# Performance work log

Measured on AMD Instinct MI355X. Metric: run time of the kernel, lower is better.

Reference implementation:

```python
import jax, jax.numpy as jnp
import numpy as np

B, L, D_MODEL, H = 2, 2048, 1024, 16
HD = D_MODEL // H  # head dim = 64


def setup_inputs() -> dict:
    key = jax.random.key(0)
    ks = jax.random.split(key, 11)
    s = 1.0 / np.sqrt(D_MODEL)
    inp = {
        "Q": jax.random.normal(ks[0], (B, L, D_MODEL), jnp.float32),
        "K": jax.random.normal(ks[1], (B, L, D_MODEL), jnp.float32),
        "V": jax.random.normal(ks[2], (B, L, D_MODEL), jnp.float32),
        "Wq": jax.random.normal(ks[3], (D_MODEL, D_MODEL), jnp.float32) * s,
        "bq": jnp.zeros((D_MODEL,), jnp.float32),
        "Wk": jax.random.normal(ks[4], (D_MODEL, D_MODEL), jnp.float32) * s,
        "bk": jnp.zeros((D_MODEL,), jnp.float32),
        "Wv": jax.random.normal(ks[5], (D_MODEL, D_MODEL), jnp.float32) * s,
        "bv": jnp.zeros((D_MODEL,), jnp.float32),
        "Wo": jax.random.normal(ks[6], (D_MODEL, D_MODEL), jnp.float32) * s,
        "bo": jnp.zeros((D_MODEL,), jnp.float32),
    }
    return inp


def _split_heads(x):
    # [B, L, H*D] -> [B, H, L, D]
    return x.reshape(B, L, H, HD).transpose(0, 2, 1, 3)


def reference(Q, K, V, Wq, bq, Wk, bk, Wv, bv, Wo, bo):
    q = _split_heads(Q @ Wq.T + bq)
    k = _split_heads(K @ Wk.T + bk)
    v = _split_heads(V @ Wv.T + bv)
    scale = 1.0 / jnp.sqrt(jnp.asarray(HD, q.dtype))
    # full [B, H, L, L] score matrix, as in the original bmm->softmax->bmm
    scores = jnp.einsum("bhqd,bhkd->bhqk", q, k) * scale
    attn = jax.nn.softmax(scores, axis=-1)
    o = jnp.einsum("bhqk,bhkd->bhqd", attn, v)
    o = o.transpose(0, 2, 1, 3).reshape(B, L, D_MODEL)  # concat heads
    return o @ Wo.T + bo
```

## Files before the change

### kernel.cpp

```cpp
#include <hip/hip_runtime.h>
#include <math.h>
#include <stdint.h>

typedef __bf16 bf16_t;
typedef __attribute__((ext_vector_type(2))) __bf16 bf16x2;
typedef __attribute__((ext_vector_type(8))) __bf16 bf16x8;
typedef __attribute__((ext_vector_type(4))) float f32x4;
typedef __attribute__((ext_vector_type(16))) float f32x16;
typedef __attribute__((address_space(1))) unsigned int gu32;
typedef __attribute__((address_space(3))) unsigned int lu32;

#define MFMA16(a, b, c) __builtin_amdgcn_mfma_f32_16x16x32_bf16((a), (b), (c), 0, 0, 0)
#define MFMA32(a, b, c) __builtin_amdgcn_mfma_f32_32x32x16_bf16((a), (b), (c), 0, 0, 0)

__device__ __forceinline__ void gll16(const void* g, void* l) {
    __builtin_amdgcn_global_load_lds((const gu32*)(uintptr_t)g,
                                     (lu32*)(uintptr_t)l, 16, 0, 0);
}

__device__ __forceinline__ bf16x8 ld_frag68(const bf16_t* p) {
    union { bf16x8 v; uint2 u[2]; } r;
    r.u[0] = *(const uint2*)p;
    r.u[1] = *(const uint2*)(p + 4);
    return r.v;
}

__global__ __launch_bounds__(256) void convert_all(
    const float* __restrict__ Q, const float* __restrict__ K, const float* __restrict__ V,
    const float* __restrict__ Wq, const float* __restrict__ Wk, const float* __restrict__ Wv,
    const float* __restrict__ Wo, bf16_t* __restrict__ dst) {
    size_t e0 = (size_t)blockIdx.x * 2048;
    const float* src; size_t off;
    if (e0 < 4194304)       { src = Q;  off = e0; }
    else if (e0 < 8388608)  { src = K;  off = e0 - 4194304; }
    else if (e0 < 12582912) { src = V;  off = e0 - 8388608; }
    else if (e0 < 13631488) { src = Wq; off = e0 - 12582912; }
    else if (e0 < 14680064) { src = Wk; off = e0 - 13631488; }
    else if (e0 < 15728640) { src = Wv; off = e0 - 14680064; }
    else                    { src = Wo; off = e0 - 15728640; }
#pragma unroll
    for (int p = 0; p < 2; ++p) {
        int t = p * 1024 + threadIdx.x * 4;
        float4 v = *(const float4*)(src + off + t);
        union { ushort4 u; bf16_t h[4]; } pk;
        pk.h[0] = (bf16_t)v.x; pk.h[1] = (bf16_t)v.y;
        pk.h[2] = (bf16_t)v.z; pk.h[3] = (bf16_t)v.w;
        *(ushort4*)(dst + e0 + t) = pk.u;
    }
}

__global__ __launch_bounds__(256) void qkv_gemm(
    const bf16_t* __restrict__ Qb, const bf16_t* __restrict__ Kb, const bf16_t* __restrict__ Vb,
    const bf16_t* __restrict__ Wqb, const bf16_t* __restrict__ Wkb, const bf16_t* __restrict__ Wvb,
    const float* __restrict__ bq, const float* __restrict__ bk, const float* __restrict__ bv,
    bf16_t* __restrict__ qo, bf16_t* __restrict__ ko, bf16_t* __restrict__ vT) {
    constexpr int Kdim = 1024, N = 1024;
    __shared__ __attribute__((aligned(16))) bf16_t smem[2 * 128 * 64];
    bf16_t* As = smem;
    bf16_t* Bs = smem + 128 * 64;

    const int tid = threadIdx.x, wave = tid >> 6, lane = tid & 63;
    const int z = blockIdx.z;
    const bf16_t* A = (z == 0) ? Qb : (z == 1) ? Kb : Vb;
    const bf16_t* W = (z == 0) ? Wqb : (z == 1) ? Wkb : Wvb;
    const float* bias = (z == 0) ? bq : (z == 1) ? bk : bv;
    const int bm = blockIdx.x * 128, bn = blockIdx.y * 128;
    const int l16 = lane & 15, quad = lane >> 4;
    const int wm = (wave >> 1) * 64, wn = (wave & 1) * 64;
    const int grow = lane >> 3, gcol = (lane & 7) * 8;

    f32x4 acc[4][4] = {};

    for (int k0 = 0; k0 < Kdim; k0 += 64) {
#pragma unroll
        for (int j = 0; j < 4; ++j) {
            int chunk = wave * 4 + j;
            int row = chunk * 8 + grow;
            gll16(A + (size_t)(bm + row) * Kdim + k0 + gcol, As + chunk * 512);
            gll16(W + (size_t)(bn + row) * Kdim + k0 + gcol, Bs + chunk * 512);
        }
        __syncthreads();
#pragma unroll
        for (int ks = 0; ks < 64; ks += 32) {
            bf16x8 af[4], bf[4];
#pragma unroll
            for (int i = 0; i < 4; ++i)
                af[i] = *(const bf16x8*)&As[(wm + i * 16 + l16) * 64 + ks + quad * 8];
#pragma unroll
            for (int i = 0; i < 4; ++i)
                bf[i] = *(const bf16x8*)&Bs[(wn + i * 16 + l16) * 64 + ks + quad * 8];
#pragma unroll
            for (int i = 0; i < 4; ++i)
#pragma unroll
                for (int j = 0; j < 4; ++j)
                    acc[i][j] = MFMA16(af[i], bf[j], acc[i][j]);
        }
        __syncthreads();
    }

    if (z < 2) {
        bf16_t* outp = (z == 0) ? qo : ko;
        const float sc = (z == 0) ? 0.18033688011112042f : 1.0f;
        constexpr int RST = 132;
#pragma unroll
        for (int p = 0; p < 2; ++p) {
            __syncthreads();
            if ((wave >> 1) == p) {
#pragma unroll
                for (int mi = 0; mi < 4; ++mi)
#pragma unroll
                    for (int nj = 0; nj < 4; ++nj) {
                        int col = wn + nj * 16 + l16;
                        float bv_ = bias[bn + col];
#pragma unroll
                        for (int r = 0; r < 4; ++r) {
                            int rp = mi * 16 + quad * 4 + r;
                            smem[rp * RST + col] = (bf16_t)((acc[mi][nj][r] + bv_) * sc);
                        }
                    }
            }
            __syncthreads();
            int rp = tid >> 2;
            int cb = (tid & 3) * 32;
            int row = bm + p * 64 + rp;
            int srow = row;
            if (z == 1) {
                int w = row & 63;
                srow = (row & ~63) | ((w & 1) ? 32 + (w >> 1) : (w >> 1));
            }
#pragma unroll
            for (int j = 0; j < 4; ++j) {
                uint2 lo = *(const uint2*)&smem[rp * RST + cb + j * 8];
                uint2 hi = *(const uint2*)&smem[rp * RST + cb + j * 8 + 4];
                *(uint4*)&outp[(size_t)srow * N + bn + cb + j * 8] =
                    make_uint4(lo.x, lo.y, hi.x, hi.y);
            }
        }
    } else {
#pragma unroll
        for (int mi = 0; mi < 4; ++mi)
#pragma unroll
            for (int nj = 0; nj < 4; ++nj) {
                int col = bn + wn + nj * 16 + l16;
                int h = col >> 6, d = col & 63;
                float bv_ = bias[col];
                int row0 = bm + wm + mi * 16 + quad * 4;
                int bb = row0 >> 11, l = row0 & 2047;
                union { ushort4 u; bf16_t h4[4]; } pk;
#pragma unroll
                for (int r = 0; r < 4; ++r) pk.h4[r] = (bf16_t)(acc[mi][nj][r] + bv_);
                *(ushort4*)&vT[(((size_t)bb * 16 + h) * 64 + d) * 2048 + l] = pk.u;
            }
    }
}

__global__ __launch_bounds__(256) void out_gemm(const bf16_t* __restrict__ A,
                                                const bf16_t* __restrict__ W,
                                                const float* __restrict__ bias,
                                                float* __restrict__ out) {
    constexpr int Kdim = 1024, N = 1024;
    __shared__ __attribute__((aligned(16))) bf16_t As[64 * 64];
    __shared__ __attribute__((aligned(16))) bf16_t Bs[128 * 64];
    const int tid = threadIdx.x, wave = tid >> 6, lane = tid & 63;
    const int bm = blockIdx.x * 64, bn = blockIdx.y * 128;
    const int l16 = lane & 15, quad = lane >> 4;
    const int wm = (wave >> 1) * 32, wn = (wave & 1) * 64;
    const int grow = lane >> 3, gcol = (lane & 7) * 8;
    f32x4 acc[2][4] = {};

    for (int k0 = 0; k0 < Kdim; k0 += 64) {
#pragma unroll
        for (int j = 0; j < 2; ++j) {
            int chunk = wave * 2 + j;
            int row = chunk * 8 + grow;
            gll16(A + (size_t)(bm + row) * Kdim + k0 + gcol, As + chunk * 512);
        }
#pragma unroll
        for (int j = 0; j < 4; ++j) {
            int chunk = wave * 4 + j;
            int row = chunk * 8 + grow;
            gll16(W + (size_t)(bn + row) * Kdim + k0 + gcol, Bs + chunk * 512);
        }
        __syncthreads();
#pragma unroll
        for (int ks = 0; ks < 64; ks += 32) {
            bf16x8 af[2], bf[4];
#pragma unroll
            for (int i = 0; i < 2; ++i)
                af[i] = *(const bf16x8*)&As[(wm + i * 16 + l16) * 64 + ks + quad * 8];
#pragma unroll
            for (int i = 0; i < 4; ++i)
                bf[i] = *(const bf16x8*)&Bs[(wn + i * 16 + l16) * 64 + ks + quad * 8];
#pragma unroll
            for (int i = 0; i < 2; ++i)
#pragma unroll
                for (int j = 0; j < 4; ++j)
                    acc[i][j] = MFMA16(af[i], bf[j], acc[i][j]);
        }
        __syncthreads();
    }
#pragma unroll
    for (int mi = 0; mi < 2; ++mi)
#pragma unroll
        for (int nj = 0; nj < 4; ++nj) {
            int col = bn + wn + nj * 16 + l16;
            float bv_ = bias[col];
#pragma unroll
            for (int r = 0; r < 4; ++r) {
                int row = bm + wm + mi * 16 + quad * 4 + r;
                out[(size_t)row * N + col] = acc[mi][nj][r] + bv_;
            }
        }
}

__global__ __launch_bounds__(256, 4) void attn5(const bf16_t* __restrict__ qo,
                                                const bf16_t* __restrict__ ko,
                                                const bf16_t* __restrict__ vT,
                                                bf16_t* __restrict__ Op,
                                                float* __restrict__ lpp) {
    constexpr int L = 2048, D = 1024, ST = 68;
    __shared__ __attribute__((aligned(16))) bf16_t ksm[64 * ST];
    __shared__ __attribute__((aligned(16))) bf16_t vsm[64 * ST];
    __shared__ __attribute__((aligned(16))) bf16_t psm[4][32 * ST];

    const int tid = threadIdx.x, wave = tid >> 6, lane = tid & 63;
    const int l31 = lane & 31, hi = lane >> 5;
    const int b = blockIdx.x >> 4, h = blockIdx.x & 15;
    const int q0 = blockIdx.y * 128;
    const int split = blockIdx.z;
    bf16_t* pw = psm[wave];
    bf16_t* Opart = Op + (size_t)split * 4194304;
    float* lpart = lpp + split * 65536;

    const int rloc = tid >> 2, cg = tid & 3;
    const bf16_t* kbase = ko + ((size_t)b * L + rloc) * D + h * 64 + cg * 16;
    const bf16_t* vbase = vT + (((size_t)b * 16 + h) * 64 + rloc) * L + cg * 16;

    bf16x8 qf[4];
    {
        const bf16_t* qptr = qo + ((size_t)b * L + q0 + wave * 32 + l31) * D + h * 64 + hi * 8;
#pragma unroll
        for (int ks = 0; ks < 4; ++ks) qf[ks] = *(const bf16x8*)(qptr + ks * 16);
    }

    f32x16 o0{}, o1{};
    float lp[16];
#pragma unroll
    for (int r = 0; r < 16; ++r) lp[r] = 0.f;

    const int kt0 = split * 16, kt1 = kt0 + 16;
    for (int kt = kt0; kt < kt1; ++kt) {
        const size_t koff = (size_t)(kt * 64) * D;
        const int voff = kt * 64;
        uint4 ka = *(const uint4*)(kbase + koff);
        uint4 kc = *(const uint4*)(kbase + koff + 8);
        uint4 va = *(const uint4*)(vbase + voff);
        uint4 vc = *(const uint4*)(vbase + voff + 8);
        __syncthreads();
        {
            bf16_t* kd = &ksm[rloc * ST + cg * 16];
            bf16_t* vd = &vsm[rloc * ST + cg * 16];
            *(uint2*)(kd + 0)  = make_uint2(ka.x, ka.y);
            *(uint2*)(kd + 4)  = make_uint2(ka.z, ka.w);
            *(uint2*)(kd + 8)  = make_uint2(kc.x, kc.y);
            *(uint2*)(kd + 12) = make_uint2(kc.z, kc.w);
            *(uint2*)(vd + 0)  = make_uint2(va.x, va.y);
            *(uint2*)(vd + 4)  = make_uint2(va.z, va.w);
            *(uint2*)(vd + 8)  = make_uint2(vc.x, vc.y);
            *(uint2*)(vd + 12) = make_uint2(vc.z, vc.w);
        }
        __syncthreads();

        f32x16 s0{}, s1{};
#pragma unroll
        for (int ks = 0; ks < 4; ++ks) {
            bf16x8 b0 = ld_frag68(&ksm[l31 * ST + ks * 16 + hi * 8]);
            bf16x8 b1 = ld_frag68(&ksm[(32 + l31) * ST + ks * 16 + hi * 8]);
            s0 = MFMA32(qf[ks], b0, s0);
            s1 = MFMA32(qf[ks], b1, s1);
        }

#pragma unroll
        for (int r = 0; r < 16; ++r) {
            int row = (r & 3) + 8 * (r >> 2) + 4 * hi;
            float p0 = exp2f(s0[r]);
            float p1 = exp2f(s1[r]);
            lp[r] += p0 + p1;
            *(bf16x2*)&pw[row * ST + 2 * l31] = bf16x2{(bf16_t)p0, (bf16_t)p1};
        }

#pragma unroll
        for (int ks = 0; ks < 4; ++ks) {
            bf16x8 a  = ld_frag68(&pw[l31 * ST + ks * 16 + hi * 8]);
            bf16x8 b0 = ld_frag68(&vsm[l31 * ST + ks * 16 + hi * 8]);
            bf16x8 b1 = ld_frag68(&vsm[(32 + l31) * ST + ks * 16 + hi * 8]);
            o0 = MFMA32(a, b0, o0);
            o1 = MFMA32(a, b1, o1);
        }
    }

#pragma unroll
    for (int r = 0; r < 16; ++r) {
        lp[r] += __shfl_xor(lp[r], 1, 64);
        lp[r] += __shfl_xor(lp[r], 2, 64);
        lp[r] += __shfl_xor(lp[r], 4, 64);
        lp[r] += __shfl_xor(lp[r], 8, 64);
        lp[r] += __shfl_xor(lp[r], 16, 64);
    }

#pragma unroll
    for (int r = 0; r < 16; ++r) {
        int row = (r & 3) + 8 * (r >> 2) + 4 * hi;
        size_t base = ((size_t)b * L + q0 + wave * 32 + row) * D + h * 64;
        Opart[base + l31] = (bf16_t)o0[r];
        Opart[base + 32 + l31] = (bf16_t)o1[r];
        if (l31 == 0)
            lpart[((size_t)b * 16 + h) * 2048 + q0 + wave * 32 + row] = lp[r];
    }
}

__global__ __launch_bounds__(256) void combine(const bf16_t* __restrict__ Op,
                                               const float* __restrict__ lpp,
                                               bf16_t* __restrict__ Ob) {
    const size_t c = (size_t)blockIdx.x * 256 + threadIdx.x;
    const int bl = (int)(c >> 7);
    const int h = ((int)c >> 3) & 15;
    const int bb = bl >> 11, l = bl & 2047;
    const int li = (bb * 16 + h) * 2048 + l;
    const float inv = 1.f / (lpp[li] + lpp[65536 + li]);
    union { uint4 u; bf16_t h8[8]; } a, b, o;
    a.u = *(const uint4*)(Op + c * 8);
    b.u = *(const uint4*)(Op + 4194304 + c * 8);
#pragma unroll
    for (int i = 0; i < 8; ++i)
        o.h8[i] = (bf16_t)(((float)a.h8[i] + (float)b.h8[i]) * inv);
    *(uint4*)(Ob + c * 8) = o.u;
}

extern "C" void kernel_launch(void* const* d_in, const int* in_sizes, int n_in,
                              void* d_out, int out_size, void* d_ws, size_t ws_size,
                              hipStream_t stream) {
    const float* Q  = (const float*)d_in[0];
    const float* Kx = (const float*)d_in[1];
    const float* V  = (const float*)d_in[2];
    const float* Wq = (const float*)d_in[3];
    const float* bq = (const float*)d_in[4];
    const float* Wk = (const float*)d_in[5];
    const float* bk = (const float*)d_in[6];
    const float* Wv = (const float*)d_in[7];
    const float* bv = (const float*)d_in[8];
    const float* Wo = (const float*)d_in[9];
    const float* bo = (const float*)d_in[10];

    bf16_t* ws0 = (bf16_t*)d_ws;
    bf16_t* Qb  = ws0;
    bf16_t* Kb  = ws0 + 4194304;
    bf16_t* Vb  = ws0 + 8388608;
    bf16_t* Wqb = ws0 + 12582912;
    bf16_t* Wkb = ws0 + 13631488;
    bf16_t* Wvb = ws0 + 14680064;
    bf16_t* Wob = ws0 + 15728640;
    bf16_t* vT  = ws0 + 16777216;
    bf16_t* Op  = Qb;
    bf16_t* Obf = Vb;
    float*  lpp = (float*)Wqb;
    bf16_t* qo = (bf16_t*)d_out;
    bf16_t* ko = qo + 4194304;

    convert_all<<<8192, 256, 0, stream>>>(Q, Kx, V, Wq, Wk, Wv, Wo, ws0);
    qkv_gemm<<<dim3(32, 8, 3), 256, 0, stream>>>(Qb, Kb, Vb, Wqb, Wkb, Wvb,
                                                 bq, bk, bv, qo, ko, vT);
    attn5<<<dim3(32, 16, 2), 256, 0, stream>>>(qo, ko, vT, Op, lpp);
    combine<<<2048, 256, 0, stream>>>(Op, lpp, Obf);
    out_gemm<<<dim3(64, 8), 256, 0, stream>>>(Obf, Wob, bo, (float*)d_out);
}
```

Measured before the change: 249.5 us.

## Compute transposed scores so P stays in registers, dropping the LDS round-trip

The attention kernel now computes S^T = K·Q^T by swapping the MFMA operands, so each lane holds the scores for one query row. The exponentiated probabilities can then be packed directly into the B operand of the P·V MFMA instead of being written to and re-read from a per-wave LDS buffer. The V^T layout is permuted in the QKV GEMM epilogue to match the register order, and the earlier Q/K row permutation is removed. The row-sum reduction collapses to a single shuffle, and the output is transposed through LDS so it can be stored with coalesced 16-byte writes. This removes the P LDS traffic and its shared memory, at the cost of an extra store-staging pass and layout coupling between kernels.

```diff
diff --git a/kernel.cpp b/kernel.cpp
--- a/kernel.cpp
+++ b/kernel.cpp
@@ -123,16 +123,11 @@
             int rp = tid >> 2;
             int cb = (tid & 3) * 32;
             int row = bm + p * 64 + rp;
-            int srow = row;
-            if (z == 1) {
-                int w = row & 63;
-                srow = (row & ~63) | ((w & 1) ? 32 + (w >> 1) : (w >> 1));
-            }
 #pragma unroll
             for (int j = 0; j < 4; ++j) {
                 uint2 lo = *(const uint2*)&smem[rp * RST + cb + j * 8];
                 uint2 hi = *(const uint2*)&smem[rp * RST + cb + j * 8 + 4];
-                *(uint4*)&outp[(size_t)srow * N + bn + cb + j * 8] =
+                *(uint4*)&outp[(size_t)row * N + bn + cb + j * 8] =
                     make_uint4(lo.x, lo.y, hi.x, hi.y);
             }
         }
@@ -146,10 +141,11 @@
                 float bv_ = bias[col];
                 int row0 = bm + wm + mi * 16 + quad * 4;
                 int bb = row0 >> 11, l = row0 & 2047;
+                int lb = (l & ~12) | ((l & 4) << 1) | ((l & 8) >> 1);
                 union { ushort4 u; bf16_t h4[4]; } pk;
 #pragma unroll
                 for (int r = 0; r < 4; ++r) pk.h4[r] = (bf16_t)(acc[mi][nj][r] + bv_);
-                *(ushort4*)&vT[(((size_t)bb * 16 + h) * 64 + d) * 2048 + l] = pk.u;
+                *(ushort4*)&vT[(((size_t)bb * 16 + h) * 64 + d) * 2048 + lb] = pk.u;
             }
     }
 }
@@ -213,22 +209,21 @@
         }
 }
 
-__global__ __launch_bounds__(256, 4) void attn5(const bf16_t* __restrict__ qo,
+__global__ __launch_bounds__(256, 4) void attn6(const bf16_t* __restrict__ qo,
                                                 const bf16_t* __restrict__ ko,
                                                 const bf16_t* __restrict__ vT,
                                                 bf16_t* __restrict__ Op,
                                                 float* __restrict__ lpp) {
     constexpr int L = 2048, D = 1024, ST = 68;
-    __shared__ __attribute__((aligned(16))) bf16_t ksm[64 * ST];
-    __shared__ __attribute__((aligned(16))) bf16_t vsm[64 * ST];
-    __shared__ __attribute__((aligned(16))) bf16_t psm[4][32 * ST];
+    __shared__ __attribute__((aligned(16))) bf16_t smem[2 * 64 * ST];
+    bf16_t* ksm = smem;
+    bf16_t* vsm = smem + 64 * ST;
 
     const int tid = threadIdx.x, wave = tid >> 6, lane = tid & 63;
     const int l31 = lane & 31, hi = lane >> 5;
     const int b = blockIdx.x >> 4, h = blockIdx.x & 15;
     const int q0 = blockIdx.y * 128;
     const int split = blockIdx.z;
-    bf16_t* pw = psm[wave];
     bf16_t* Opart = Op + (size_t)split * 4194304;
     float* lpart = lpp + split * 65536;
 
@@ -244,9 +239,7 @@
     }
 
     f32x16 o0{}, o1{};
-    float lp[16];
-#pragma unroll
-    for (int r = 0; r < 16; ++r) lp[r] = 0.f;
+    float lpl = 0.f;
 
     const int kt0 = split * 16, kt1 = kt0 + 16;
     for (int kt = kt0; kt < kt1; ++kt) {
@@ -274,48 +267,49 @@
         f32x16 s0{}, s1{};
 #pragma unroll
         for (int ks = 0; ks < 4; ++ks) {
-            bf16x8 b0 = ld_frag68(&ksm[l31 * ST + ks * 16 + hi * 8]);
-            bf16x8 b1 = ld_frag68(&ksm[(32 + l31) * ST + ks * 16 + hi * 8]);
-            s0 = MFMA32(qf[ks], b0, s0);
-            s1 = MFMA32(qf[ks], b1, s1);
-        }
-
-#pragma unroll
-        for (int r = 0; r < 16; ++r) {
-            int row = (r & 3) + 8 * (r >> 2) + 4 * hi;
-            float p0 = exp2f(s0[r]);
-            float p1 = exp2f(s1[r]);
-            lp[r] += p0 + p1;
-            *(bf16x2*)&pw[row * ST + 2 * l31] = bf16x2{(bf16_t)p0, (bf16_t)p1};
-        }
-
-#pragma unroll
-        for (int ks = 0; ks < 4; ++ks) {
-            bf16x8 a  = ld_frag68(&pw[l31 * ST + ks * 16 + hi * 8]);
-            bf16x8 b0 = ld_frag68(&vsm[l31 * ST + ks * 16 + hi * 8]);
-            bf16x8 b1 = ld_frag68(&vsm[(32 + l31) * ST + ks * 16 + hi * 8]);
-            o0 = MFMA32(a, b0, o0);
-            o1 = MFMA32(a, b1, o1);
-        }
-    }
-
-#pragma unroll
-    for (int r = 0; r < 16; ++r) {
-        lp[r] += __shfl_xor(lp[r], 1, 64);
-        lp[r] += __shfl_xor(lp[r], 2, 64);
-        lp[r] += __shfl_xor(lp[r], 4, 64);
-        lp[r] += __shfl_xor(lp[r], 8, 64);
-        lp[r] += __shfl_xor(lp[r], 16, 64);
-    }
-
-#pragma unroll
-    for (int r = 0; r < 16; ++r) {
-        int row = (r & 3) + 8 * (r >> 2) + 4 * hi;
-        size_t base = ((size_t)b * L + q0 + wave * 32 + row) * D + h * 64;
-        Opart[base + l31] = (bf16_t)o0[r];
-        Opart[base + 32 + l31] = (bf16_t)o1[r];
-        if (l31 == 0)
-            lpart[((size_t)b * 16 + h) * 2048 + q0 + wave * 32 + row] = lp[r];
+            bf16x8 k0 = ld_frag68(&ksm[l31 * ST + ks * 16 + hi * 8]);
+            bf16x8 k1 = ld_frag68(&ksm[(32 + l31) * ST + ks * 16 + hi * 8]);
+            s0 = MFMA32(k0, qf[ks], s0);
+            s1 = MFMA32(k1, qf[ks], s1);
+        }
+
+#pragma unroll
+        for (int t = 0; t < 4; ++t) {
+            union { bf16x8 v; bf16_t e[8]; } pf;
+#pragma unroll
+            for (int j = 0; j < 8; ++j) {
+                float sv = (t < 2) ? s0[(t & 1) * 8 + j] : s1[(t & 1) * 8 + j];
+                float p = __builtin_amdgcn_exp2f(sv);
+                lpl += p;
+                pf.e[j] = (bf16_t)p;
+            }
+            bf16x8 v0 = ld_frag68(&vsm[l31 * ST + t * 16 + hi * 8]);
+            bf16x8 v1 = ld_frag68(&vsm[(32 + l31) * ST + t * 16 + hi * 8]);
+            o0 = MFMA32(v0, pf.v, o0);
+            o1 = MFMA32(v1, pf.v, o1);
+        }
+    }
+
+    lpl += __shfl_xor(lpl, 32, 64);
+    if (hi == 0)
+        lpart[((size_t)b * 16 + h) * 2048 + q0 + wave * 32 + l31] = lpl;
+
+    __syncthreads();
+    bf16_t* ew = smem + wave * (32 * ST);
+#pragma unroll
+    for (int r = 0; r < 16; r += 2) {
+        int d = (r & 3) + 8 * (r >> 2) + 4 * hi;
+        *(bf16x2*)&ew[l31 * ST + d] = bf16x2{(bf16_t)o0[r], (bf16_t)o0[r + 1]};
+        *(bf16x2*)&ew[l31 * ST + 32 + d] = bf16x2{(bf16_t)o1[r], (bf16_t)o1[r + 1]};
+    }
+#pragma unroll
+    for (int p = 0; p < 4; ++p) {
+        int rr = p * 8 + (lane >> 3);
+        int cc = (lane & 7) * 8;
+        uint2 lo = *(const uint2*)&ew[rr * ST + cc];
+        uint2 hi2 = *(const uint2*)&ew[rr * ST + cc + 4];
+        *(uint4*)&Opart[((size_t)b * L + q0 + wave * 32 + rr) * D + h * 64 + cc] =
+            make_uint4(lo.x, lo.y, hi2.x, hi2.y);
     }
 }
 
@@ -370,7 +364,7 @@
     convert_all<<<8192, 256, 0, stream>>>(Q, Kx, V, Wq, Wk, Wv, Wo, ws0);
     qkv_gemm<<<dim3(32, 8, 3), 256, 0, stream>>>(Qb, Kb, Vb, Wqb, Wkb, Wvb,
                                                  bq, bk, bv, qo, ko, vT);
-    attn5<<<dim3(32, 16, 2), 256, 0, stream>>>(qo, ko, vT, Op, lpp);
+    attn6<<<dim3(32, 16, 2), 256, 0, stream>>>(qo, ko, vT, Op, lpp);
     combine<<<2048, 256, 0, stream>>>(Op, lpp, Obf);
     out_gemm<<<dim3(64, 8), 256, 0, stream>>>(Obf, Wob, bo, (float*)d_out);
 }
```

Result: faster. 234.1 us (-6.2%).
